# Performance work log

Hardware: AMD Instinct MI355X
Metric: run time of the kernel (lower is better)

## Reference

```python
import jax, jax.numpy as jnp
import numpy as np
import math

B, S, D, H = 2, 2048, 1024, 16
DK = D // H

def setup_inputs() -> dict:
    key = jax.random.key(0)
    ks = jax.random.split(key, 12)
    s = 1.0 / math.sqrt(D)
    inp = {
        'input_q': jax.random.normal(ks[0], (B, S, D), jnp.float32),
        'input_k': jax.random.normal(ks[1], (B, S, D), jnp.float32),
        'input_v': jax.random.normal(ks[2], (B, S, D), jnp.float32),
        'mask': jax.random.randint(ks[3], (B, 1, S, S), 0, 2, jnp.int32),
        'Wq': jax.random.normal(ks[4], (D, D), jnp.float32) * s,
        'bq': jnp.zeros((D,), jnp.float32),
        'Wk': jax.random.normal(ks[5], (D, D), jnp.float32) * s,
        'bk': jnp.zeros((D,), jnp.float32),
        'Wv': jax.random.normal(ks[6], (D, D), jnp.float32) * s,
        'bv': jnp.zeros((D,), jnp.float32),
        'Wo': jax.random.normal(ks[7], (D, D), jnp.float32) * s,
        'bo': jnp.zeros((D,), jnp.float32),
    }
    return inp

def reference(input_q, input_k, input_v, mask, Wq, bq, Wk, bk, Wv, bv, Wo, bo):
    # Linear projections (torch Linear: x @ W.T + b), split into heads: [B,H,S,DK]
    q = (input_q @ Wq.T + bq).reshape(B, S, H, DK).transpose(0, 2, 1, 3)
    k = (input_k @ Wk.T + bk).reshape(B, S, H, DK).transpose(0, 2, 1, 3)
    v = (input_v @ Wv.T + bv).reshape(B, S, H, DK).transpose(0, 2, 1, 3)
    scores = jnp.einsum('bhqd,bhkd->bhqk', q, k) / math.sqrt(DK)
    scores = jnp.where(mask == 0, jnp.float32(-1e9), scores)
    attn = jax.nn.softmax(scores, axis=-1)
    out = jnp.einsum('bhqk,bhkd->bhqd', attn, v)
    out = out.transpose(0, 2, 1, 3).reshape(B, S, D)
    return out @ Wo.T + bo
```

## Files before the change

### kernel.cpp

```cpp
#include <hip/hip_runtime.h>
#include <math.h>

#define kB 2
#define kS 2048
#define kD 1024
#define kH 16
#define kM (kB * kS)

typedef unsigned short u16;
typedef unsigned int u32;
typedef unsigned long long u64;
typedef short s16x8 __attribute__((ext_vector_type(8)));
typedef float f32x4 __attribute__((ext_vector_type(4)));

__device__ __forceinline__ u16 f2bf(float f) {
    u32 u = __float_as_uint(f);
    u += 0x7FFFu + ((u >> 16) & 1u);
    return (u16)(u >> 16);
}

__device__ __forceinline__ u32 pack_bf2(float f0, float f1) {
    const u32 r0 = __float_as_uint(f0) + 0x8000u;
    const u32 r1 = __float_as_uint(f1) + 0x8000u;
    return __builtin_amdgcn_perm(r1, r0, 0x07060302u);
}

typedef __attribute__((address_space(1))) void as1_void;
typedef __attribute__((address_space(3))) void as3_void;
__device__ __forceinline__ void async_copy16(const void* g, void* l) {
    __builtin_amdgcn_global_load_lds((as1_void*)(unsigned long long)g,
                                     (as3_void*)(unsigned)(unsigned long long)l,
                                     16, 0, 0);
}

__global__ __launch_bounds__(256) void prep(
        const float* __restrict__ xq, const float* __restrict__ xk, const float* __restrict__ xv,
        const float* __restrict__ Wq, const float* __restrict__ Wk,
        const float* __restrict__ Wv, const float* __restrict__ Wo,
        const int* __restrict__ msk,
        u16* __restrict__ xqb, u16* __restrict__ xkb, u16* __restrict__ xvb,
        u16* __restrict__ wqb, u16* __restrict__ wkb, u16* __restrict__ wvb,
        u16* __restrict__ wob, u64* __restrict__ prepM) {
    const int bid = blockIdx.x;
    const int tid = threadIdx.x;
    if (bid < 16384) {
        const float* in;
        u16* out;
        int i;
        if (bid < 12288) {
            const int z = bid >> 12;
            in = z == 0 ? xq : (z == 1 ? xk : xv);
            out = z == 0 ? xqb : (z == 1 ? xkb : xvb);
            i = (bid & 4095) * 256 + tid;
        } else {
            const int z = (bid - 12288) >> 10;
            in = z == 0 ? Wq : (z == 1 ? Wk : (z == 2 ? Wv : Wo));
            out = z == 0 ? wqb : (z == 1 ? wkb : (z == 2 ? wvb : wob));
            i = ((bid - 12288) & 1023) * 256 + tid;
        }
        const float4 v = ((const float4*)in)[i];
        ushort4 o;
        o.x = f2bf(v.x); o.y = f2bf(v.y); o.z = f2bf(v.z); o.w = f2bf(v.w);
        ((ushort4*)out)[i] = o;
    } else {
        const int wid = (bid - 16384) * 4 + (tid >> 6);
        const int lane = tid & 63;
        const int kt = wid & 31, qb = (wid >> 5) & 127, b = wid >> 12;
        const int q = qb * 16 + (lane & 15);
        const int kbase = kt * 64 + ((lane >> 4) << 2);
        const int* mrow = msk + ((size_t)b * kS + q) * kS;
        u64 keep = 0;
#pragma unroll
        for (int e = 0; e < 16; ++e) {
            const int k = kbase + (e >> 2) * 16 + (e & 3);
            const u64 bl = __ballot(mrow[k] != 0);
            if (lane == e) keep = bl;
        }
        if (lane < 16)
            prepM[(((size_t)b * 128 + qb) * 32 + kt) * 16 + lane] = keep;
    }
}

template <int MODE>
__device__ __forceinline__ void gemm_bt_body(const u16* __restrict__ A,
                                             const u16* __restrict__ W,
                                             const float* __restrict__ bias,
                                             void* __restrict__ Cp) {
    __shared__ u16 As[128 * 32];
    __shared__ u16 Bs[128 * 32];
    const int tid = threadIdx.x;
    const int wave = tid >> 6, lane = tid & 63;
    const int l15 = lane & 15, quad = lane >> 4;
    const int wr = wave >> 1, wc = wave & 1;
    const int m0 = (MODE == 3 ? blockIdx.x : blockIdx.y) * 128;
    const int n0 = (MODE == 3 ? blockIdx.y : blockIdx.x) * 128;

    const int srow = lane >> 2;
    const int schk = (lane & 3) ^ (srow & 3);
    const u16* gA0 = A + (size_t)(m0 + 32 * wave + srow) * kD + schk * 8;
    const u16* gA1 = gA0 + 16 * kD;
    const u16* gB0 = W + (size_t)(n0 + 32 * wave + srow) * kD + schk * 8;
    const u16* gB1 = gB0 + 16 * kD;
    u16* lA0 = As + (32 * wave) * 32;
    u16* lA1 = lA0 + 16 * 32;
    u16* lB0 = Bs + (32 * wave) * 32;
    u16* lB1 = lB0 + 16 * 32;

    const int rdoff = (quad ^ (l15 & 3)) * 8;

    f32x4 acc[4][4];
#pragma unroll
    for (int i = 0; i < 4; ++i)
#pragma unroll
        for (int j = 0; j < 4; ++j) acc[i][j] = (f32x4)0.f;

    for (int kt = 0; kt < kD; kt += 32) {
        __syncthreads();
        async_copy16(gA0 + kt, lA0);
        async_copy16(gA1 + kt, lA1);
        async_copy16(gB0 + kt, lB0);
        async_copy16(gB1 + kt, lB1);
        __syncthreads();

        s16x8 af[4], bf[4];
#pragma unroll
        for (int fm = 0; fm < 4; ++fm)
            af[fm] = *(const s16x8*)(As + (wr * 64 + fm * 16 + l15) * 32 + rdoff);
#pragma unroll
        for (int fn = 0; fn < 4; ++fn)
            bf[fn] = *(const s16x8*)(Bs + (wc * 64 + fn * 16 + l15) * 32 + rdoff);
#pragma unroll
        for (int fm = 0; fm < 4; ++fm)
#pragma unroll
            for (int fn = 0; fn < 4; ++fn)
                acc[fm][fn] = __builtin_amdgcn_mfma_f32_16x16x32_bf16(
                    af[fm], bf[fn], acc[fm][fn], 0, 0, 0);
    }

    if constexpr (MODE == 3) {
#pragma unroll
        for (int fn = 0; fn < 4; ++fn) {
            const int sglob = n0 + wc * 64 + fn * 16 + l15;
            const int bb = sglob >> 11, ss = sglob & (kS - 1);
#pragma unroll
            for (int fm = 0; fm < 4; ++fm) {
                const int dglob = m0 + wr * 64 + fm * 16 + quad * 4;
                const float4 b4 = *(const float4*)(bias + dglob);
                const float bb4[4] = {b4.x, b4.y, b4.z, b4.w};
                const int hh = dglob >> 6, dd = dglob & 63;
                u16* base = (u16*)Cp + ((size_t)(bb * kH + hh) * 64 + dd) * kS + ss;
#pragma unroll
                for (int r = 0; r < 4; ++r)
                    base[(size_t)r * kS] = f2bf(acc[fm][fn][r] + bb4[r]);
            }
        }
    } else {
#pragma unroll
        for (int fn = 0; fn < 4; ++fn) {
            const int col = n0 + wc * 64 + fn * 16 + l15;
            const float bv = bias[col];
#pragma unroll
            for (int fm = 0; fm < 4; ++fm) {
                const int row = m0 + wr * 64 + fm * 16 + quad * 4;
#pragma unroll
                for (int r = 0; r < 4; ++r) {
                    const float v = acc[fm][fn][r] + bv;
                    if constexpr (MODE == 0)
                        ((u16*)Cp)[(size_t)(row + r) * kD + col] = f2bf(v);
                    else
                        ((float*)Cp)[(size_t)(row + r) * kD + col] = v;
                }
            }
        }
    }
}

__global__ __launch_bounds__(256) void qkv_gemm(
        const u16* __restrict__ xq, const u16* __restrict__ xk, const u16* __restrict__ xv,
        const u16* __restrict__ wq, const u16* __restrict__ wk, const u16* __restrict__ wv,
        const float* __restrict__ bq, const float* __restrict__ bk, const float* __restrict__ bv,
        u16* __restrict__ q, u16* __restrict__ k, u16* __restrict__ vt) {
    const int z = blockIdx.z;
    if (z == 0)      gemm_bt_body<0>(xq, wq, bq, q);
    else if (z == 1) gemm_bt_body<0>(xk, wk, bk, k);
    else             gemm_bt_body<3>(wv, xv, bv, vt);
}

__global__ __launch_bounds__(256) void o_gemm(const u16* __restrict__ A,
                                              const u16* __restrict__ W,
                                              const float* __restrict__ bias,
                                              float* __restrict__ C) {
    gemm_bt_body<2>(A, W, bias, C);
}

#define kC 0.180336880f

__global__ __launch_bounds__(256) void attn_mfma(const u16* __restrict__ Qb,
                                                 const u16* __restrict__ Kb,
                                                 const u16* __restrict__ Vt,
                                                 const u64* __restrict__ prepM,
                                                 u16* __restrict__ Ob) {
    __shared__ u16 Qs[64 * 64];
    __shared__ u16 Ks[64 * 64];
    __shared__ u16 Vs[64 * 64];
    __shared__ u16 Ps[64 * 64];

    const int tid = threadIdx.x;
    const int wave = tid >> 6, lane = tid & 63;
    const int l15 = lane & 15, quad = lane >> 4, l7 = lane & 7;
    const int q0 = blockIdx.x * 64;
    const int b = blockIdx.y >> 4, h = blockIdx.y & 15;

    const int srow = lane >> 3;
    const int schk = l7 ^ srow;

    {
        const u16* g0 = Qb + ((size_t)(b * kS + q0 + 16 * wave + srow)) * kD + h * 64 + schk * 8;
        async_copy16(g0, Qs + (16 * wave) * 64);
        async_copy16(g0 + 8 * kD, Qs + (16 * wave + 8) * 64);
    }
    const u16* gK0 = Kb + ((size_t)(b * kS + 16 * wave + srow)) * kD + h * 64 + schk * 8;
    const u16* gV0 = Vt + ((size_t)((b * kH + h) * 64 + 16 * wave + srow)) * kS + schk * 8;

    const int wave_u = __builtin_amdgcn_readfirstlane(wave);
    const u64* mbase = prepM + (((size_t)b * 128 + blockIdx.x * 4 + wave_u) * 32) * 16;

    f32x4 oacc[4];
#pragma unroll
    for (int i = 0; i < 4; ++i) oacc[i] = (f32x4)0.f;
    float l_r = 0.f;

    __syncthreads();
    s16x8 bq[2];
    bq[0] = *(const s16x8*)(Qs + (16 * wave + l15) * 64 + ((0 + quad) ^ l7) * 8);
    bq[1] = *(const s16x8*)(Qs + (16 * wave + l15) * 64 + ((4 + quad) ^ l7) * 8);
    u16* psrow = Ps + (16 * wave + l15) * 64;

    for (int kt = 0; kt < kS; kt += 64) {
        __syncthreads();
        async_copy16(gK0 + (size_t)kt * kD, Ks + (16 * wave) * 64);
        async_copy16(gK0 + (size_t)(kt + 8) * kD, Ks + (16 * wave + 8) * 64);
        async_copy16(gV0 + kt, Vs + (16 * wave) * 64);
        async_copy16(gV0 + 8 * kS + kt, Vs + (16 * wave + 8) * 64);
        __syncthreads();

        f32x4 s[4];
#pragma unroll
        for (int fn = 0; fn < 4; ++fn) s[fn] = (f32x4)0.f;
#pragma unroll
        for (int kc = 0; kc < 2; ++kc)
#pragma unroll
            for (int fn = 0; fn < 4; ++fn) {
                const s16x8 ak = *(const s16x8*)(Ks + (fn * 16 + l15) * 64 + ((kc * 4 + quad) ^ l7) * 8);
                s[fn] = __builtin_amdgcn_mfma_f32_16x16x32_bf16(ak, bq[kc], s[fn], 0, 0, 0);
            }

        const u64* mt = mbase + (kt >> 6) * 16;
        float ps = 0.f;
#pragma unroll
        for (int fn = 0; fn < 4; ++fn)
#pragma unroll
            for (int r = 0; r < 4; ++r) {
                const u64 mm = mt[fn * 4 + r];
                const float p = exp2f(fmaf(s[fn][r], kC, -8.0f));
                float pm;
                asm("v_cndmask_b32 %0, 0, %1, %2" : "=v"(pm) : "v"(p), "s"(mm));
                s[fn][r] = pm;
                ps += pm;
            }
        ps += __shfl_xor(ps, 16);
        ps += __shfl_xor(ps, 32);
        l_r += ps;

#pragma unroll
        for (int fn = 0; fn < 4; ++fn) {
            uint2 o;
            o.x = pack_bf2(s[fn][0], s[fn][1]);
            o.y = pack_bf2(s[fn][2], s[fn][3]);
            const int chunk = fn * 2 + (quad >> 1);
            *(uint2*)(psrow + ((chunk ^ l7) * 8) + (quad & 1) * 4) = o;
        }

#pragma unroll
        for (int kc = 0; kc < 2; ++kc) {
            const s16x8 bp = *(const s16x8*)(psrow + ((kc * 4 + quad) ^ l7) * 8);
#pragma unroll
            for (int fd = 0; fd < 4; ++fd) {
                const s16x8 av = *(const s16x8*)(Vs + (fd * 16 + l15) * 64 + ((kc * 4 + quad) ^ l7) * 8);
                oacc[fd] = __builtin_amdgcn_mfma_f32_16x16x32_bf16(av, bp, oacc[fd], 0, 0, 0);
            }
        }
    }

    const float inv = 1.f / l_r;
    const size_t orow = (size_t)(b * kS + q0 + 16 * wave + l15);
#pragma unroll
    for (int fd = 0; fd < 4; ++fd) {
        uint2 o;
        o.x = pack_bf2(oacc[fd][0] * inv, oacc[fd][1] * inv);
        o.y = pack_bf2(oacc[fd][2] * inv, oacc[fd][3] * inv);
        *(uint2*)(Ob + orow * kD + h * 64 + fd * 16 + quad * 4) = o;
    }
}

extern "C" void kernel_launch(void* const* d_in, const int* in_sizes, int n_in,
                              void* d_out, int out_size, void* d_ws, size_t ws_size,
                              hipStream_t stream) {
    const float* xq = (const float*)d_in[0];
    const float* xk = (const float*)d_in[1];
    const float* xv = (const float*)d_in[2];
    const int*  msk = (const int*)d_in[3];
    const float* Wq = (const float*)d_in[4];
    const float* bq = (const float*)d_in[5];
    const float* Wk = (const float*)d_in[6];
    const float* bk = (const float*)d_in[7];
    const float* Wv = (const float*)d_in[8];
    const float* bv = (const float*)d_in[9];
    const float* Wo = (const float*)d_in[10];
    const float* bo = (const float*)d_in[11];
    float* out = (float*)d_out;

    const size_t NX = (size_t)kM * kD;
    const size_t NW = (size_t)kD * kD;

    u64* prepM = (u64*)d_ws;
    u16* p = (u16*)((char*)d_ws + (1 << 20));
    u16* xqb = p; p += NX;
    u16* xkb = p; p += NX;
    u16* xvb = p; p += NX;
    u16* wqb = p; p += NW;
    u16* wkb = p; p += NW;
    u16* wvb = p; p += NW;
    u16* wob = p; p += NW;
    u16* qb  = p; p += NX;
    u16* kb  = p; p += NX;
    u16* vtb = p; p += NX;
    u16* ab  = xqb;

    prep<<<18432, 256, 0, stream>>>(xq, xk, xv, Wq, Wk, Wv, Wo, msk,
                                    xqb, xkb, xvb, wqb, wkb, wvb, wob, prepM);

    dim3 gq(kD / 128, kM / 128, 3);
    qkv_gemm<<<gq, 256, 0, stream>>>(xqb, xkb, xvb, wqb, wkb, wvb, bq, bk, bv, qb, kb, vtb);

    dim3 ga(kS / 64, kB * kH);
    attn_mfma<<<ga, 256, 0, stream>>>(qb, kb, vtb, prepM, ab);

    dim3 go(kD / 128, kM / 128);
    o_gemm<<<go, 256, 0, stream>>>(ab, wob, bo, out);
}
```

Baseline: 291.1 us.

## Repack mask per query row, deepen GEMM K-tile, load V directly, MFMA row sums

```diff
diff --git a/kernel.cpp b/kernel.cpp
--- a/kernel.cpp
+++ b/kernel.cpp
@@ -40,7 +40,7 @@
         const int* __restrict__ msk,
         u16* __restrict__ xqb, u16* __restrict__ xkb, u16* __restrict__ xvb,
         u16* __restrict__ wqb, u16* __restrict__ wkb, u16* __restrict__ wvb,
-        u16* __restrict__ wob, u64* __restrict__ prepM) {
+        u16* __restrict__ wob, u64* __restrict__ mb) {
     const int bid = blockIdx.x;
     const int tid = threadIdx.x;
     if (bid < 16384) {
@@ -65,19 +65,10 @@
     } else {
         const int wid = (bid - 16384) * 4 + (tid >> 6);
         const int lane = tid & 63;
-        const int kt = wid & 31, qb = (wid >> 5) & 127, b = wid >> 12;
-        const int q = qb * 16 + (lane & 15);
-        const int kbase = kt * 64 + ((lane >> 4) << 2);
-        const int* mrow = msk + ((size_t)b * kS + q) * kS;
-        u64 keep = 0;
-#pragma unroll
-        for (int e = 0; e < 16; ++e) {
-            const int k = kbase + (e >> 2) * 16 + (e & 3);
-            const u64 bl = __ballot(mrow[k] != 0);
-            if (lane == e) keep = bl;
-        }
-        if (lane < 16)
-            prepM[(((size_t)b * 128 + qb) * 32 + kt) * 16 + lane] = keep;
+        const int b = wid >> 16, q = (wid >> 5) & 2047, t = wid & 31;
+        const int v = msk[((size_t)b * kS + q) * kS + t * 64 + lane];
+        const u64 bits = __ballot(v != 0);
+        if (lane == 0) mb[((size_t)b * 32 + t) * kS + q] = bits;
     }
 }
 
@@ -86,27 +77,21 @@
                                              const u16* __restrict__ W,
                                              const float* __restrict__ bias,
                                              void* __restrict__ Cp) {
-    __shared__ u16 As[128 * 32];
-    __shared__ u16 Bs[128 * 32];
+    __shared__ u16 As[128 * 64];
+    __shared__ u16 Bs[128 * 64];
     const int tid = threadIdx.x;
     const int wave = tid >> 6, lane = tid & 63;
-    const int l15 = lane & 15, quad = lane >> 4;
+    const int l15 = lane & 15, quad = lane >> 4, l7 = lane & 7;
     const int wr = wave >> 1, wc = wave & 1;
     const int m0 = (MODE == 3 ? blockIdx.x : blockIdx.y) * 128;
     const int n0 = (MODE == 3 ? blockIdx.y : blockIdx.x) * 128;
 
-    const int srow = lane >> 2;
-    const int schk = (lane & 3) ^ (srow & 3);
-    const u16* gA0 = A + (size_t)(m0 + 32 * wave + srow) * kD + schk * 8;
-    const u16* gA1 = gA0 + 16 * kD;
-    const u16* gB0 = W + (size_t)(n0 + 32 * wave + srow) * kD + schk * 8;
-    const u16* gB1 = gB0 + 16 * kD;
-    u16* lA0 = As + (32 * wave) * 32;
-    u16* lA1 = lA0 + 16 * 32;
-    u16* lB0 = Bs + (32 * wave) * 32;
-    u16* lB1 = lB0 + 16 * 32;
-
-    const int rdoff = (quad ^ (l15 & 3)) * 8;
+    const int srow = lane >> 3;
+    const int schk = l7 ^ srow;
+    const u16* gA = A + (size_t)(m0 + 32 * wave + srow) * kD + schk * 8;
+    const u16* gB = W + (size_t)(n0 + 32 * wave + srow) * kD + schk * 8;
+    u16* lA = As + (32 * wave) * 64;
+    u16* lB = Bs + (32 * wave) * 64;
 
     f32x4 acc[4][4];
 #pragma unroll
@@ -114,27 +99,32 @@
 #pragma unroll
         for (int j = 0; j < 4; ++j) acc[i][j] = (f32x4)0.f;
 
-    for (int kt = 0; kt < kD; kt += 32) {
+    for (int kt = 0; kt < kD; kt += 64) {
         __syncthreads();
-        async_copy16(gA0 + kt, lA0);
-        async_copy16(gA1 + kt, lA1);
-        async_copy16(gB0 + kt, lB0);
-        async_copy16(gB1 + kt, lB1);
+#pragma unroll
+        for (int i = 0; i < 4; ++i) {
+            async_copy16(gA + (size_t)(8 * i) * kD + kt, lA + (8 * i) * 64);
+            async_copy16(gB + (size_t)(8 * i) * kD + kt, lB + (8 * i) * 64);
+        }
         __syncthreads();
 
-        s16x8 af[4], bf[4];
-#pragma unroll
-        for (int fm = 0; fm < 4; ++fm)
-            af[fm] = *(const s16x8*)(As + (wr * 64 + fm * 16 + l15) * 32 + rdoff);
-#pragma unroll
-        for (int fn = 0; fn < 4; ++fn)
-            bf[fn] = *(const s16x8*)(Bs + (wc * 64 + fn * 16 + l15) * 32 + rdoff);
-#pragma unroll
-        for (int fm = 0; fm < 4; ++fm)
+#pragma unroll
+        for (int s = 0; s < 2; ++s) {
+            const int rdoff = ((s * 4 + quad) ^ l7) * 8;
+            s16x8 af[4], bf[4];
+#pragma unroll
+            for (int fm = 0; fm < 4; ++fm)
+                af[fm] = *(const s16x8*)(As + (wr * 64 + fm * 16 + l15) * 64 + rdoff);
 #pragma unroll
             for (int fn = 0; fn < 4; ++fn)
-                acc[fm][fn] = __builtin_amdgcn_mfma_f32_16x16x32_bf16(
-                    af[fm], bf[fn], acc[fm][fn], 0, 0, 0);
+                bf[fn] = *(const s16x8*)(Bs + (wc * 64 + fn * 16 + l15) * 64 + rdoff);
+#pragma unroll
+            for (int fm = 0; fm < 4; ++fm)
+#pragma unroll
+                for (int fn = 0; fn < 4; ++fn)
+                    acc[fm][fn] = __builtin_amdgcn_mfma_f32_16x16x32_bf16(
+                        af[fm], bf[fn], acc[fm][fn], 0, 0, 0);
+        }
     }
 
     if constexpr (MODE == 3) {
@@ -198,12 +188,10 @@
 __global__ __launch_bounds__(256) void attn_mfma(const u16* __restrict__ Qb,
                                                  const u16* __restrict__ Kb,
                                                  const u16* __restrict__ Vt,
-                                                 const u64* __restrict__ prepM,
+                                                 const u64* __restrict__ mb,
                                                  u16* __restrict__ Ob) {
-    __shared__ u16 Qs[64 * 64];
+    __shared__ u16 QPs[64 * 64];
     __shared__ u16 Ks[64 * 64];
-    __shared__ u16 Vs[64 * 64];
-    __shared__ u16 Ps[64 * 64];
 
     const int tid = threadIdx.x;
     const int wave = tid >> 6, lane = tid & 63;
@@ -216,32 +204,43 @@
 
     {
         const u16* g0 = Qb + ((size_t)(b * kS + q0 + 16 * wave + srow)) * kD + h * 64 + schk * 8;
-        async_copy16(g0, Qs + (16 * wave) * 64);
-        async_copy16(g0 + 8 * kD, Qs + (16 * wave + 8) * 64);
-    }
-    const u16* gK0 = Kb + ((size_t)(b * kS + 16 * wave + srow)) * kD + h * 64 + schk * 8;
-    const u16* gV0 = Vt + ((size_t)((b * kH + h) * 64 + 16 * wave + srow)) * kS + schk * 8;
-
-    const int wave_u = __builtin_amdgcn_readfirstlane(wave);
-    const u64* mbase = prepM + (((size_t)b * 128 + blockIdx.x * 4 + wave_u) * 32) * 16;
+        async_copy16(g0, QPs + (16 * wave) * 64);
+        async_copy16(g0 + 8 * kD, QPs + (16 * wave + 8) * 64);
+    }
+    const u16* gK = Kb + ((size_t)(b * kS + 16 * wave + srow)) * kD + h * 64 + schk * 8;
+    const u16* gVf = Vt + ((size_t)((b * kH + h) * 64 + l15)) * kS + quad * 8;
+    const u64* mrow = mb + (size_t)b * 32 * kS + (q0 + 16 * wave + l15);
 
     f32x4 oacc[4];
 #pragma unroll
     for (int i = 0; i < 4; ++i) oacc[i] = (f32x4)0.f;
-    float l_r = 0.f;
+    f32x4 lacc = (f32x4)0.f;
+
+    s16x8 ones;
+#pragma unroll
+    for (int j = 0; j < 8; ++j) ones[j] = (short)0x3F80;
 
     __syncthreads();
-    s16x8 bq[2];
-    bq[0] = *(const s16x8*)(Qs + (16 * wave + l15) * 64 + ((0 + quad) ^ l7) * 8);
-    bq[1] = *(const s16x8*)(Qs + (16 * wave + l15) * 64 + ((4 + quad) ^ l7) * 8);
-    u16* psrow = Ps + (16 * wave + l15) * 64;
-
-    for (int kt = 0; kt < kS; kt += 64) {
+    s16x8 qf[2];
+    qf[0] = *(const s16x8*)(QPs + (16 * wave + l15) * 64 + ((0 + quad) ^ l7) * 8);
+    qf[1] = *(const s16x8*)(QPs + (16 * wave + l15) * 64 + ((4 + quad) ^ l7) * 8);
+    u16* psrow = QPs + (16 * wave + l15) * 64;
+
+    for (int t = 0; t < kS / 64; ++t) {
+        const int kt = t * 64;
+
+        s16x8 av[2][4];
+#pragma unroll
+        for (int kc = 0; kc < 2; ++kc)
+#pragma unroll
+            for (int fd = 0; fd < 4; ++fd)
+                av[kc][fd] = *(const s16x8*)(gVf + (size_t)(fd * 16) * kS + kt + kc * 32);
+        const u64 m64 = mrow[(size_t)t * kS];
+        const u32 klo = (u32)m64, khi = (u32)(m64 >> 32);
+
         __syncthreads();
-        async_copy16(gK0 + (size_t)kt * kD, Ks + (16 * wave) * 64);
-        async_copy16(gK0 + (size_t)(kt + 8) * kD, Ks + (16 * wave + 8) * 64);
-        async_copy16(gV0 + kt, Vs + (16 * wave) * 64);
-        async_copy16(gV0 + 8 * kS + kt, Vs + (16 * wave + 8) * 64);
+        async_copy16(gK + (size_t)kt * kD, Ks + (16 * wave) * 64);
+        async_copy16(gK + (size_t)(kt + 8) * kD, Ks + (16 * wave + 8) * 64);
         __syncthreads();
 
         f32x4 s[4];
@@ -251,48 +250,39 @@
         for (int kc = 0; kc < 2; ++kc)
 #pragma unroll
             for (int fn = 0; fn < 4; ++fn) {
-                const s16x8 ak = *(const s16x8*)(Ks + (fn * 16 + l15) * 64 + ((kc * 4 + quad) ^ l7) * 8);
-                s[fn] = __builtin_amdgcn_mfma_f32_16x16x32_bf16(ak, bq[kc], s[fn], 0, 0, 0);
+                const s16x8 ak = *(const s16x8*)(Ks + (fn * 16 + l15) * 64 +
+                                                 ((kc * 4 + quad) ^ l7) * 8);
+                s[fn] = __builtin_amdgcn_mfma_f32_16x16x32_bf16(ak, qf[kc], s[fn], 0, 0, 0);
             }
 
-        const u64* mt = mbase + (kt >> 6) * 16;
-        float ps = 0.f;
-#pragma unroll
-        for (int fn = 0; fn < 4; ++fn)
+#pragma unroll
+        for (int fn = 0; fn < 4; ++fn) {
+            const u32 w32 = (fn & 2) ? khi : klo;
+            const u32 sh = (fn & 1) * 16 + quad * 4;
+            float p[4];
 #pragma unroll
             for (int r = 0; r < 4; ++r) {
-                const u64 mm = mt[fn * 4 + r];
-                const float p = exp2f(fmaf(s[fn][r], kC, -8.0f));
-                float pm;
-                asm("v_cndmask_b32 %0, 0, %1, %2" : "=v"(pm) : "v"(p), "s"(mm));
-                s[fn][r] = pm;
-                ps += pm;
+                p[r] = exp2f(fmaf(s[fn][r], kC, -8.0f));
+                p[r] *= (float)((w32 >> (sh + r)) & 1u);
             }
-        ps += __shfl_xor(ps, 16);
-        ps += __shfl_xor(ps, 32);
-        l_r += ps;
-
-#pragma unroll
-        for (int fn = 0; fn < 4; ++fn) {
             uint2 o;
-            o.x = pack_bf2(s[fn][0], s[fn][1]);
-            o.y = pack_bf2(s[fn][2], s[fn][3]);
-            const int chunk = fn * 2 + (quad >> 1);
-            *(uint2*)(psrow + ((chunk ^ l7) * 8) + (quad & 1) * 4) = o;
+            o.x = pack_bf2(p[0], p[1]);
+            o.y = pack_bf2(p[2], p[3]);
+            *(uint2*)(psrow + ((fn * 2 + (quad >> 1)) ^ l7) * 8 + (quad & 1) * 4) = o;
         }
 
 #pragma unroll
         for (int kc = 0; kc < 2; ++kc) {
             const s16x8 bp = *(const s16x8*)(psrow + ((kc * 4 + quad) ^ l7) * 8);
-#pragma unroll
-            for (int fd = 0; fd < 4; ++fd) {
-                const s16x8 av = *(const s16x8*)(Vs + (fd * 16 + l15) * 64 + ((kc * 4 + quad) ^ l7) * 8);
-                oacc[fd] = __builtin_amdgcn_mfma_f32_16x16x32_bf16(av, bp, oacc[fd], 0, 0, 0);
-            }
-        }
-    }
-
-    const float inv = 1.f / l_r;
+            lacc = __builtin_amdgcn_mfma_f32_16x16x32_bf16(ones, bp, lacc, 0, 0, 0);
+#pragma unroll
+            for (int fd = 0; fd < 4; ++fd)
+                oacc[fd] = __builtin_amdgcn_mfma_f32_16x16x32_bf16(
+                    av[kc][fd], bp, oacc[fd], 0, 0, 0);
+        }
+    }
+
+    const float inv = 1.f / lacc[0];
     const size_t orow = (size_t)(b * kS + q0 + 16 * wave + l15);
 #pragma unroll
     for (int fd = 0; fd < 4; ++fd) {
@@ -323,7 +313,7 @@
     const size_t NX = (size_t)kM * kD;
     const size_t NW = (size_t)kD * kD;
 
-    u64* prepM = (u64*)d_ws;
+    u64* mb = (u64*)d_ws;
     u16* p = (u16*)((char*)d_ws + (1 << 20));
     u16* xqb = p; p += NX;
     u16* xkb = p; p += NX;
@@ -337,14 +327,14 @@
     u16* vtb = p; p += NX;
     u16* ab  = xqb;
 
-    prep<<<18432, 256, 0, stream>>>(xq, xk, xv, Wq, Wk, Wv, Wo, msk,
-                                    xqb, xkb, xvb, wqb, wkb, wvb, wob, prepM);
+    prep<<<49152, 256, 0, stream>>>(xq, xk, xv, Wq, Wk, Wv, Wo, msk,
+                                    xqb, xkb, xvb, wqb, wkb, wvb, wob, mb);
 
     dim3 gq(kD / 128, kM / 128, 3);
     qkv_gemm<<<gq, 256, 0, stream>>>(xqb, xkb, xvb, wqb, wkb, wvb, bq, bk, bv, qb, kb, vtb);
 
     dim3 ga(kS / 64, kB * kH);
-    attn_mfma<<<ga, 256, 0, stream>>>(qb, kb, vtb, prepM, ab);
+    attn_mfma<<<ga, 256, 0, stream>>>(qb, kb, vtb, mb, ab);
 
     dim3 go(kD / 128, kM / 128);
     o_gemm<<<go, 256, 0, stream>>>(ab, wob, bo, out);
```

Measured after the change: 372.3 us. +27.9%, slower.
